# Kernel optimization log

Hardware: AMD Instinct MI355X
Metric: run time of the kernel (lower is better)

The kernel has to match this reference:

```python
import jax, jax.numpy as jnp
import numpy as np

N = 100000      # nodes
E = 1600000     # edges (avg degree 16)
F_IN = 256
F_OUT = 128


def setup_inputs() -> dict:
    key = jax.random.key(0)
    k1, k2, k3, k4, k5 = jax.random.split(key, 5)
    x = jax.random.normal(k1, (N, F_IN), dtype=jnp.float32)
    adj_row = jax.random.randint(k2, (E,), 0, N, dtype=jnp.int32)
    adj_col = jax.random.randint(k3, (E,), 0, N, dtype=jnp.int32)
    adj_vals = jax.random.uniform(k4, (E,), dtype=jnp.float32)
    # he_uniform init for weight, zeros for bias (as in build())
    limit = jnp.sqrt(6.0 / F_IN)
    w = jax.random.uniform(k5, (F_IN, F_OUT), minval=-limit, maxval=limit, dtype=jnp.float32)
    b = jnp.zeros((F_OUT,), dtype=jnp.float32)
    return {"x": x, "adj_row": adj_row, "adj_col": adj_col, "adj_vals": adj_vals, "w": w, "b": b}


def reference(x, adj_row, adj_col, adj_vals, w, b):
    # dense feature transform: [N, F_in] @ [F_in, F_out] -> [N, F_out]
    h = x @ w
    # sparse adjacency SpMM (COO): out[r] += vals[e] * h[c] for edge e=(r,c)
    msgs = adj_vals[:, None] * h[adj_col]            # [E, F_out]
    agg = jax.ops.segment_sum(msgs, adj_row, num_segments=N)  # [N, F_out]
    # bias + relu activation
    return jax.nn.relu(agg + b)
```

## Files before the change

kernel.cpp:

```cpp
#include <hip/hip_runtime.h>
#include <hip/hip_bf16.h>
#include <cstdint>
#include <cstddef>

#define N_NODES 100000
#define N_EDGES 1600000
#define F_IN 256
#define F_OUT 128

#define NB 1563
#define NBLK 196
#define TILE 8192
#define CAP 1536

typedef __attribute__((ext_vector_type(8))) short short8;
typedef __attribute__((ext_vector_type(4))) float floatx4;

static __device__ __forceinline__ unsigned short f2bf(float f) {
    union { float f; unsigned u; } v; v.f = f;
    unsigned r = v.u + 0x7FFF + ((v.u >> 16) & 1);
    return (unsigned short)(r >> 16);
}

__global__ void prep_w(const float* __restrict__ w, unsigned short* __restrict__ wT) {
    int i = blockIdx.x * 256 + threadIdx.x;
    int k = i >> 7;
    int n = i & 127;
    int g = (k >> 3) ^ (n & 7);
    wT[n * 256 + g * 8 + (k & 7)] = f2bf(w[i]);
}

__global__ __launch_bounds__(256, 2) void gemm_xw(const float* __restrict__ x,
                                                  const unsigned short* __restrict__ wT,
                                                  unsigned short* __restrict__ h) {
    __shared__ __align__(16) unsigned short wlds[128 * 256];
    const int tid = threadIdx.x;
    {
        const floatx4* src = reinterpret_cast<const floatx4*>(wT);
        floatx4* dst = reinterpret_cast<floatx4*>(wlds);
        #pragma unroll
        for (int i = 0; i < 16; i++) dst[tid + i * 256] = src[tid + i * 256];
    }
    __syncthreads();

    const int wave = tid >> 6, lane = tid & 63;
    const int quad = lane >> 4, l16 = lane & 15;
    const int rowbase = blockIdx.x * 256 + wave * 64;

    floatx4 acc[4][8];
    #pragma unroll
    for (int mf = 0; mf < 4; mf++)
        #pragma unroll
        for (int nt = 0; nt < 8; nt++) acc[mf][nt] = (floatx4)0.f;

    #pragma unroll
    for (int ks = 0; ks < 8; ks++) {
        const int k0 = ks * 32 + quad * 8;
        short8 afrag[4];
        #pragma unroll
        for (int mf = 0; mf < 4; mf++) {
            int row = rowbase + mf * 16 + l16;
            if (row >= N_NODES) row = N_NODES - 1;
            const float* xp = x + (size_t)row * F_IN + k0;
            floatx4 x0 = *reinterpret_cast<const floatx4*>(xp);
            floatx4 x1 = *reinterpret_cast<const floatx4*>(xp + 4);
            short8 a;
            a[0] = (short)f2bf(x0[0]); a[1] = (short)f2bf(x0[1]);
            a[2] = (short)f2bf(x0[2]); a[3] = (short)f2bf(x0[3]);
            a[4] = (short)f2bf(x1[0]); a[5] = (short)f2bf(x1[1]);
            a[6] = (short)f2bf(x1[2]); a[7] = (short)f2bf(x1[3]);
            afrag[mf] = a;
        }
        short8 bfrag[8];
        const int gq = ks * 4 + quad;
        #pragma unroll
        for (int nt = 0; nt < 8; nt++) {
            const int n = nt * 16 + l16;
            const int g = gq ^ (n & 7);
            bfrag[nt] = *reinterpret_cast<const short8*>(&wlds[n * 256 + g * 8]);
        }
        #pragma unroll
        for (int mf = 0; mf < 4; mf++)
            #pragma unroll
            for (int nt = 0; nt < 8; nt++)
                acc[mf][nt] = __builtin_amdgcn_mfma_f32_16x16x32_bf16(
                    afrag[mf], bfrag[nt], acc[mf][nt], 0, 0, 0);
    }

    #pragma unroll
    for (int mf = 0; mf < 4; mf++) {
        const int mbase = rowbase + mf * 16 + quad * 4;
        #pragma unroll
        for (int reg = 0; reg < 4; reg++) {
            const int m = mbase + reg;
            if (m < N_NODES) {
                short8 hv;
                #pragma unroll
                for (int nt = 0; nt < 8; nt++) hv[nt] = (short)f2bf(acc[mf][nt][reg]);
                *reinterpret_cast<short8*>(&h[(size_t)m * F_OUT + l16 * 8]) = hv;
            }
        }
    }
}

__global__ __launch_bounds__(256) void bucket_hist(const int* __restrict__ row,
                                                   int* __restrict__ bucket_total,
                                                   int* __restrict__ blockbase) {
    __shared__ int hist[NB];
    const int t = threadIdx.x, blk = blockIdx.x;
    for (int i = t; i < NB; i += 256) hist[i] = 0;
    __syncthreads();
    const long tb = (long)blk * TILE;
    #pragma unroll
    for (int c = 0; c < 8; c++) {
        long i0 = tb + c * 1024 + t * 4;
        if (i0 + 4 <= N_EDGES) {
            int4 r = *reinterpret_cast<const int4*>(row + i0);
            atomicAdd(&hist[r.x >> 6], 1); atomicAdd(&hist[r.y >> 6], 1);
            atomicAdd(&hist[r.z >> 6], 1); atomicAdd(&hist[r.w >> 6], 1);
        } else {
            for (long i = i0; i < N_EDGES && i < i0 + 4; i++)
                atomicAdd(&hist[row[i] >> 6], 1);
        }
    }
    __syncthreads();
    for (int bin = t; bin < NB; bin += 256)
        blockbase[bin * NBLK + blk] = atomicAdd(&bucket_total[bin], hist[bin]);
}

__global__ void bucket_scan(const int* __restrict__ bucket_total,
                            int* __restrict__ bucket_base) {
    const int lane = threadIdx.x;
    int loc[25];
    int s = 0;
    #pragma unroll
    for (int k = 0; k < 25; k++) {
        int idx = lane * 25 + k;
        int v = (idx < NB) ? bucket_total[idx] : 0;
        loc[k] = s; s += v;
    }
    int run = s;
    #pragma unroll
    for (int off = 1; off < 64; off <<= 1) {
        int u = __shfl_up(run, off);
        if (lane >= off) run += u;
    }
    const int base = run - s;
    #pragma unroll
    for (int k = 0; k < 25; k++) {
        int idx = lane * 25 + k;
        if (idx <= NB) bucket_base[idx] = base + loc[k];
    }
}

__global__ __launch_bounds__(256) void bucket_scatter(const int* __restrict__ row,
                                                      const int* __restrict__ col,
                                                      const float* __restrict__ val,
                                                      const int* __restrict__ bucket_base,
                                                      const int* __restrict__ blockbase,
                                                      int2* __restrict__ metabuf) {
    __shared__ int sbase[NB];
    const int t = threadIdx.x, blk = blockIdx.x;
    for (int bin = t; bin < NB; bin += 256)
        sbase[bin] = bucket_base[bin] + blockbase[bin * NBLK + blk];
    __syncthreads();
    const long tb = (long)blk * TILE;
    #pragma unroll
    for (int c = 0; c < 8; c++) {
        long i0 = tb + c * 1024 + t * 4;
        if (i0 + 4 <= N_EDGES) {
            int4 r  = *reinterpret_cast<const int4*>(row + i0);
            int4 cc = *reinterpret_cast<const int4*>(col + i0);
            floatx4 vv = *reinterpret_cast<const floatx4*>(val + i0);
            int rr[4] = {r.x, r.y, r.z, r.w};
            int c4[4] = {cc.x, cc.y, cc.z, cc.w};
            float v4[4] = {vv[0], vv[1], vv[2], vv[3]};
            #pragma unroll
            for (int j = 0; j < 4; j++) {
                int bin = rr[j] >> 6, rl = rr[j] & 63;
                int pos = atomicAdd(&sbase[bin], 1);
                metabuf[pos] = make_int2(c4[j] | (rl << 24), __float_as_int(v4[j]));
            }
        } else {
            for (long i = i0; i < N_EDGES && i < i0 + 4; i++) {
                int rv = row[i];
                int bin = rv >> 6, rl = rv & 63;
                int pos = atomicAdd(&sbase[bin], 1);
                metabuf[pos] = make_int2(col[i] | (rl << 24), __float_as_int(val[i]));
            }
        }
    }
}

__global__ __launch_bounds__(512, 8) void spmm_fused(const unsigned short* __restrict__ h,
                                                     const int* __restrict__ bucket_base,
                                                     const int2* __restrict__ meta,
                                                     const float* __restrict__ bias,
                                                     float* __restrict__ out) {
    __shared__ int2 raw[CAP];
    __shared__ int2 ord[CAP];
    __shared__ int hist[64], startS[64], cursor[64];
    const int t = threadIdx.x, b = blockIdx.x;
    const int b0 = bucket_base[b];
    int n = bucket_base[b + 1] - b0; if (n > CAP) n = CAP;

    if (t < 64) hist[t] = 0;
    __syncthreads();
    for (int i = t; i < n; i += 512) {
        int2 e = meta[b0 + i];
        raw[i] = e;
        atomicAdd(&hist[((unsigned)e.x >> 24) & 63], 1);
    }
    __syncthreads();
    if (t < 64) {
        int h0 = hist[t];
        int s0 = h0;
        #pragma unroll
        for (int off = 1; off < 64; off <<= 1) {
            int u = __shfl_up(s0, off);
            if (t >= off) s0 += u;
        }
        startS[t] = s0 - h0; cursor[t] = s0 - h0;
    }
    __syncthreads();
    for (int i = t; i < n; i += 512) {
        int2 e = raw[i];
        int rl = ((unsigned)e.x >> 24) & 63;
        int pos = atomicAdd(&cursor[rl], 1);
        ord[pos] = make_int2(e.x & 0x00FFFFFF, e.y);
    }
    __syncthreads();

    const int lane = t & 63;
    const int l16 = lane & 15;
    const int grp = (t >> 6) * 4 + (lane >> 4);
    const unsigned short* hp = h + l16 * 8;

    #pragma unroll
    for (int j = 0; j < 2; j++) {
        const int rl = grp * 2 + j;
        const int s = startS[rl], d = hist[rl];
        float acc[8];
        #pragma unroll
        for (int k = 0; k < 8; k++) acc[k] = 0.f;
        for (int i = 0; i < d; i += 4) {
            int2 mm[4];
            #pragma unroll
            for (int u = 0; u < 4; u++) {
                int idx = i + u; if (idx > d - 1) idx = d - 1;
                mm[u] = ord[s + idx];
            }
            uint4 hv[4];
            #pragma unroll
            for (int u = 0; u < 4; u++)
                hv[u] = *reinterpret_cast<const uint4*>(hp + (size_t)mm[u].x * F_OUT);
            #pragma unroll
            for (int u = 0; u < 4; u++) {
                float v = (i + u < d) ? __int_as_float(mm[u].y) : 0.f;
                #pragma unroll
                for (int k = 0; k < 4; k++) {
                    unsigned uu = ((const unsigned*)&hv[u])[k];
                    acc[2 * k]     += v * __uint_as_float(uu << 16);
                    acc[2 * k + 1] += v * __uint_as_float(uu & 0xffff0000u);
                }
            }
        }
        const int r = b * 64 + rl;
        if (r < N_NODES) {
            float* op = out + (size_t)r * F_OUT + l16;
            #pragma unroll
            for (int jc = 0; jc < 8; jc++) {
                float o = fmaxf(acc[jc] + bias[jc * 16 + l16], 0.f);
                op[jc * 16] = o;
            }
        }
    }
}

extern "C" void kernel_launch(void* const* d_in, const int* in_sizes, int n_in,
                              void* d_out, int out_size, void* d_ws, size_t ws_size,
                              hipStream_t stream) {
    const float* x        = (const float*)d_in[0];
    const int*   adj_row  = (const int*)d_in[1];
    const int*   adj_col  = (const int*)d_in[2];
    const float* adj_vals = (const float*)d_in[3];
    const float* w        = (const float*)d_in[4];
    const float* b        = (const float*)d_in[5];
    float* out = (float*)d_out;

    char* ws = (char*)d_ws;
    unsigned short* wT = (unsigned short*)ws;
    unsigned short* h  = (unsigned short*)(ws + 65536);
    size_t off = 65536 + (size_t)N_NODES * F_OUT * 2;
    int2* metabuf  = (int2*)(ws + off);   off += (size_t)N_EDGES * 8;
    int* blockbase = (int*)(ws + off);    off += (size_t)NB * NBLK * 4;
    int* bucket_total = (int*)(ws + off); off += 8192;
    int* bucket_base  = (int*)(ws + off); off += 8192;

    prep_w<<<128, 256, 0, stream>>>(w, wT);
    hipMemsetAsync(bucket_total, 0, NB * 4, stream);
    gemm_xw<<<(N_NODES + 255) / 256, 256, 0, stream>>>(x, wT, h);
    bucket_hist<<<NBLK, 256, 0, stream>>>(adj_row, bucket_total, blockbase);
    bucket_scan<<<1, 64, 0, stream>>>(bucket_total, bucket_base);
    bucket_scatter<<<NBLK, 256, 0, stream>>>(adj_row, adj_col, adj_vals,
                                             bucket_base, blockbase, metabuf);
    spmm_fused<<<NB, 512, 0, stream>>>(h, bucket_base, metabuf, b, out);
}
```

Baseline: 304.3 us.

## Fuse GEMM and edge bucketing into one launch with fixed-capacity buckets

Replaces the separate gemm, histogram, scan and scatter kernels with one launch. The first blocks run the X·W GEMM and the remaining blocks histogram and scatter edges. Buckets now have a fixed capacity slot (CAP entries each), so the global prefix scan and per-block base table go away, and the counter reset moves into prep_w, removing the memset. This saves several launches and serialization points and lets the GEMM and the bucketing overlap. The trade-off is a larger, padded metadata buffer, and edges beyond CAP per bucket are silently dropped, though the old spmm kernel already clamped to CAP.

```diff
diff --git a/kernel.cpp b/kernel.cpp
--- a/kernel.cpp
+++ b/kernel.cpp
@@ -12,6 +12,7 @@
 #define NBLK 196
 #define TILE 8192
 #define CAP 1536
+#define GEMM_BLOCKS 391
 
 typedef __attribute__((ext_vector_type(8))) short short8;
 typedef __attribute__((ext_vector_type(4))) float floatx4;
@@ -22,178 +23,155 @@
     return (unsigned short)(r >> 16);
 }
 
-__global__ void prep_w(const float* __restrict__ w, unsigned short* __restrict__ wT) {
+__global__ void prep_w(const float* __restrict__ w, unsigned short* __restrict__ wT,
+                       int* __restrict__ cnt) {
     int i = blockIdx.x * 256 + threadIdx.x;
     int k = i >> 7;
     int n = i & 127;
     int g = (k >> 3) ^ (n & 7);
     wT[n * 256 + g * 8 + (k & 7)] = f2bf(w[i]);
-}
-
-__global__ __launch_bounds__(256, 2) void gemm_xw(const float* __restrict__ x,
-                                                  const unsigned short* __restrict__ wT,
-                                                  unsigned short* __restrict__ h) {
-    __shared__ __align__(16) unsigned short wlds[128 * 256];
+    if (blockIdx.x == 0)
+        for (int j = threadIdx.x; j < NB; j += 256) cnt[j] = 0;
+}
+
+__global__ __launch_bounds__(256, 2) void fused_mid(const float* __restrict__ x,
+                                                    const unsigned short* __restrict__ wT,
+                                                    unsigned short* __restrict__ h,
+                                                    const int* __restrict__ row,
+                                                    const int* __restrict__ col,
+                                                    const float* __restrict__ val,
+                                                    int* __restrict__ cnt,
+                                                    int2* __restrict__ metabuf) {
+    __shared__ __align__(16) unsigned short smem[128 * 256];
     const int tid = threadIdx.x;
-    {
-        const floatx4* src = reinterpret_cast<const floatx4*>(wT);
-        floatx4* dst = reinterpret_cast<floatx4*>(wlds);
-        #pragma unroll
-        for (int i = 0; i < 16; i++) dst[tid + i * 256] = src[tid + i * 256];
-    }
-    __syncthreads();
-
-    const int wave = tid >> 6, lane = tid & 63;
-    const int quad = lane >> 4, l16 = lane & 15;
-    const int rowbase = blockIdx.x * 256 + wave * 64;
-
-    floatx4 acc[4][8];
-    #pragma unroll
-    for (int mf = 0; mf < 4; mf++)
-        #pragma unroll
-        for (int nt = 0; nt < 8; nt++) acc[mf][nt] = (floatx4)0.f;
-
-    #pragma unroll
-    for (int ks = 0; ks < 8; ks++) {
-        const int k0 = ks * 32 + quad * 8;
-        short8 afrag[4];
+
+    if (blockIdx.x < GEMM_BLOCKS) {
+        unsigned short* wlds = smem;
+        {
+            const floatx4* src = reinterpret_cast<const floatx4*>(wT);
+            floatx4* dst = reinterpret_cast<floatx4*>(wlds);
+            #pragma unroll
+            for (int i = 0; i < 16; i++) dst[tid + i * 256] = src[tid + i * 256];
+        }
+        __syncthreads();
+
+        const int wave = tid >> 6, lane = tid & 63;
+        const int quad = lane >> 4, l16 = lane & 15;
+        const int rowbase = blockIdx.x * 256 + wave * 64;
+
+        floatx4 acc[4][8];
+        #pragma unroll
+        for (int mf = 0; mf < 4; mf++)
+            #pragma unroll
+            for (int nt = 0; nt < 8; nt++) acc[mf][nt] = (floatx4)0.f;
+
+        #pragma unroll
+        for (int ks = 0; ks < 8; ks++) {
+            const int k0 = ks * 32 + quad * 8;
+            short8 afrag[4];
+            #pragma unroll
+            for (int mf = 0; mf < 4; mf++) {
+                int r = rowbase + mf * 16 + l16;
+                if (r >= N_NODES) r = N_NODES - 1;
+                const float* xp = x + (size_t)r * F_IN + k0;
+                floatx4 x0 = *reinterpret_cast<const floatx4*>(xp);
+                floatx4 x1 = *reinterpret_cast<const floatx4*>(xp + 4);
+                short8 a;
+                a[0] = (short)f2bf(x0[0]); a[1] = (short)f2bf(x0[1]);
+                a[2] = (short)f2bf(x0[2]); a[3] = (short)f2bf(x0[3]);
+                a[4] = (short)f2bf(x1[0]); a[5] = (short)f2bf(x1[1]);
+                a[6] = (short)f2bf(x1[2]); a[7] = (short)f2bf(x1[3]);
+                afrag[mf] = a;
+            }
+            short8 bfrag[8];
+            const int gq = ks * 4 + quad;
+            #pragma unroll
+            for (int nt = 0; nt < 8; nt++) {
+                const int n = nt * 16 + l16;
+                const int g = gq ^ (n & 7);
+                bfrag[nt] = *reinterpret_cast<const short8*>(&wlds[n * 256 + g * 8]);
+            }
+            #pragma unroll
+            for (int mf = 0; mf < 4; mf++)
+                #pragma unroll
+                for (int nt = 0; nt < 8; nt++)
+                    acc[mf][nt] = __builtin_amdgcn_mfma_f32_16x16x32_bf16(
+                        afrag[mf], bfrag[nt], acc[mf][nt], 0, 0, 0);
+        }
+
         #pragma unroll
         for (int mf = 0; mf < 4; mf++) {
-            int row = rowbase + mf * 16 + l16;
-            if (row >= N_NODES) row = N_NODES - 1;
-            const float* xp = x + (size_t)row * F_IN + k0;
-            floatx4 x0 = *reinterpret_cast<const floatx4*>(xp);
-            floatx4 x1 = *reinterpret_cast<const floatx4*>(xp + 4);
-            short8 a;
-            a[0] = (short)f2bf(x0[0]); a[1] = (short)f2bf(x0[1]);
-            a[2] = (short)f2bf(x0[2]); a[3] = (short)f2bf(x0[3]);
-            a[4] = (short)f2bf(x1[0]); a[5] = (short)f2bf(x1[1]);
-            a[6] = (short)f2bf(x1[2]); a[7] = (short)f2bf(x1[3]);
-            afrag[mf] = a;
-        }
-        short8 bfrag[8];
-        const int gq = ks * 4 + quad;
-        #pragma unroll
-        for (int nt = 0; nt < 8; nt++) {
-            const int n = nt * 16 + l16;
-            const int g = gq ^ (n & 7);
-            bfrag[nt] = *reinterpret_cast<const short8*>(&wlds[n * 256 + g * 8]);
-        }
-        #pragma unroll
-        for (int mf = 0; mf < 4; mf++)
-            #pragma unroll
-            for (int nt = 0; nt < 8; nt++)
-                acc[mf][nt] = __builtin_amdgcn_mfma_f32_16x16x32_bf16(
-                    afrag[mf], bfrag[nt], acc[mf][nt], 0, 0, 0);
-    }
-
-    #pragma unroll
-    for (int mf = 0; mf < 4; mf++) {
-        const int mbase = rowbase + mf * 16 + quad * 4;
-        #pragma unroll
-        for (int reg = 0; reg < 4; reg++) {
-            const int m = mbase + reg;
-            if (m < N_NODES) {
-                short8 hv;
+            const int mbase = rowbase + mf * 16 + quad * 4;
+            #pragma unroll
+            for (int reg = 0; reg < 4; reg++) {
+                const int m = mbase + reg;
+                if (m < N_NODES) {
+                    short8 hv;
+                    #pragma unroll
+                    for (int nt = 0; nt < 8; nt++) hv[nt] = (short)f2bf(acc[mf][nt][reg]);
+                    *reinterpret_cast<short8*>(&h[(size_t)m * F_OUT + l16 * 8]) = hv;
+                }
+            }
+        }
+    } else {
+        int* hist   = reinterpret_cast<int*>(smem);
+        int* cursor = hist + NB;
+        const int blk = blockIdx.x - GEMM_BLOCKS;
+        for (int i = tid; i < NB; i += 256) hist[i] = 0;
+        __syncthreads();
+        const long tb = (long)blk * TILE;
+        #pragma unroll
+        for (int c = 0; c < 8; c++) {
+            long i0 = tb + c * 1024 + tid * 4;
+            if (i0 + 4 <= N_EDGES) {
+                int4 r = *reinterpret_cast<const int4*>(row + i0);
+                atomicAdd(&hist[r.x >> 6], 1); atomicAdd(&hist[r.y >> 6], 1);
+                atomicAdd(&hist[r.z >> 6], 1); atomicAdd(&hist[r.w >> 6], 1);
+            } else {
+                for (long i = i0; i < N_EDGES && i < i0 + 4; i++)
+                    atomicAdd(&hist[row[i] >> 6], 1);
+            }
+        }
+        __syncthreads();
+        for (int bin = tid; bin < NB; bin += 256) {
+            int hc = hist[bin];
+            int base = bin * CAP;
+            if (hc) base += atomicAdd(&cnt[bin], hc);
+            cursor[bin] = base;
+        }
+        __syncthreads();
+        #pragma unroll
+        for (int c = 0; c < 8; c++) {
+            long i0 = tb + c * 1024 + tid * 4;
+            if (i0 + 4 <= N_EDGES) {
+                int4 r  = *reinterpret_cast<const int4*>(row + i0);
+                int4 cc = *reinterpret_cast<const int4*>(col + i0);
+                floatx4 vv = *reinterpret_cast<const floatx4*>(val + i0);
+                int rr[4] = {r.x, r.y, r.z, r.w};
+                int c4[4] = {cc.x, cc.y, cc.z, cc.w};
+                float v4[4] = {vv[0], vv[1], vv[2], vv[3]};
                 #pragma unroll
-                for (int nt = 0; nt < 8; nt++) hv[nt] = (short)f2bf(acc[mf][nt][reg]);
-                *reinterpret_cast<short8*>(&h[(size_t)m * F_OUT + l16 * 8]) = hv;
-            }
-        }
-    }
-}
-
-__global__ __launch_bounds__(256) void bucket_hist(const int* __restrict__ row,
-                                                   int* __restrict__ bucket_total,
-                                                   int* __restrict__ blockbase) {
-    __shared__ int hist[NB];
-    const int t = threadIdx.x, blk = blockIdx.x;
-    for (int i = t; i < NB; i += 256) hist[i] = 0;
-    __syncthreads();
-    const long tb = (long)blk * TILE;
-    #pragma unroll
-    for (int c = 0; c < 8; c++) {
-        long i0 = tb + c * 1024 + t * 4;
-        if (i0 + 4 <= N_EDGES) {
-            int4 r = *reinterpret_cast<const int4*>(row + i0);
-            atomicAdd(&hist[r.x >> 6], 1); atomicAdd(&hist[r.y >> 6], 1);
-            atomicAdd(&hist[r.z >> 6], 1); atomicAdd(&hist[r.w >> 6], 1);
-        } else {
-            for (long i = i0; i < N_EDGES && i < i0 + 4; i++)
-                atomicAdd(&hist[row[i] >> 6], 1);
-        }
-    }
-    __syncthreads();
-    for (int bin = t; bin < NB; bin += 256)
-        blockbase[bin * NBLK + blk] = atomicAdd(&bucket_total[bin], hist[bin]);
-}
-
-__global__ void bucket_scan(const int* __restrict__ bucket_total,
-                            int* __restrict__ bucket_base) {
-    const int lane = threadIdx.x;
-    int loc[25];
-    int s = 0;
-    #pragma unroll
-    for (int k = 0; k < 25; k++) {
-        int idx = lane * 25 + k;
-        int v = (idx < NB) ? bucket_total[idx] : 0;
-        loc[k] = s; s += v;
-    }
-    int run = s;
-    #pragma unroll
-    for (int off = 1; off < 64; off <<= 1) {
-        int u = __shfl_up(run, off);
-        if (lane >= off) run += u;
-    }
-    const int base = run - s;
-    #pragma unroll
-    for (int k = 0; k < 25; k++) {
-        int idx = lane * 25 + k;
-        if (idx <= NB) bucket_base[idx] = base + loc[k];
-    }
-}
-
-__global__ __launch_bounds__(256) void bucket_scatter(const int* __restrict__ row,
-                                                      const int* __restrict__ col,
-                                                      const float* __restrict__ val,
-                                                      const int* __restrict__ bucket_base,
-                                                      const int* __restrict__ blockbase,
-                                                      int2* __restrict__ metabuf) {
-    __shared__ int sbase[NB];
-    const int t = threadIdx.x, blk = blockIdx.x;
-    for (int bin = t; bin < NB; bin += 256)
-        sbase[bin] = bucket_base[bin] + blockbase[bin * NBLK + blk];
-    __syncthreads();
-    const long tb = (long)blk * TILE;
-    #pragma unroll
-    for (int c = 0; c < 8; c++) {
-        long i0 = tb + c * 1024 + t * 4;
-        if (i0 + 4 <= N_EDGES) {
-            int4 r  = *reinterpret_cast<const int4*>(row + i0);
-            int4 cc = *reinterpret_cast<const int4*>(col + i0);
-            floatx4 vv = *reinterpret_cast<const floatx4*>(val + i0);
-            int rr[4] = {r.x, r.y, r.z, r.w};
-            int c4[4] = {cc.x, cc.y, cc.z, cc.w};
-            float v4[4] = {vv[0], vv[1], vv[2], vv[3]};
-            #pragma unroll
-            for (int j = 0; j < 4; j++) {
-                int bin = rr[j] >> 6, rl = rr[j] & 63;
-                int pos = atomicAdd(&sbase[bin], 1);
-                metabuf[pos] = make_int2(c4[j] | (rl << 24), __float_as_int(v4[j]));
-            }
-        } else {
-            for (long i = i0; i < N_EDGES && i < i0 + 4; i++) {
-                int rv = row[i];
-                int bin = rv >> 6, rl = rv & 63;
-                int pos = atomicAdd(&sbase[bin], 1);
-                metabuf[pos] = make_int2(col[i] | (rl << 24), __float_as_int(val[i]));
+                for (int j = 0; j < 4; j++) {
+                    int bin = rr[j] >> 6, rl = rr[j] & 63;
+                    int pos = atomicAdd(&cursor[bin], 1);
+                    if (pos < (bin + 1) * CAP)
+                        metabuf[pos] = make_int2(c4[j] | (rl << 24), __float_as_int(v4[j]));
+                }
+            } else {
+                for (long i = i0; i < N_EDGES && i < i0 + 4; i++) {
+                    int rv = row[i];
+                    int bin = rv >> 6, rl = rv & 63;
+                    int pos = atomicAdd(&cursor[bin], 1);
+                    if (pos < (bin + 1) * CAP)
+                        metabuf[pos] = make_int2(col[i] | (rl << 24), __float_as_int(val[i]));
+                }
             }
         }
     }
 }
 
 __global__ __launch_bounds__(512, 8) void spmm_fused(const unsigned short* __restrict__ h,
-                                                     const int* __restrict__ bucket_base,
+                                                     const int* __restrict__ cnt,
                                                      const int2* __restrict__ meta,
                                                      const float* __restrict__ bias,
                                                      float* __restrict__ out) {
@@ -201,8 +179,8 @@
     __shared__ int2 ord[CAP];
     __shared__ int hist[64], startS[64], cursor[64];
     const int t = threadIdx.x, b = blockIdx.x;
-    const int b0 = bucket_base[b];
-    int n = bucket_base[b + 1] - b0; if (n > CAP) n = CAP;
+    const int b0 = b * CAP;
+    int n = cnt[b]; if (n > CAP) n = CAP;
 
     if (t < 64) hist[t] = 0;
     __syncthreads();
@@ -292,17 +270,11 @@
     unsigned short* wT = (unsigned short*)ws;
     unsigned short* h  = (unsigned short*)(ws + 65536);
     size_t off = 65536 + (size_t)N_NODES * F_OUT * 2;
-    int2* metabuf  = (int2*)(ws + off);   off += (size_t)N_EDGES * 8;
-    int* blockbase = (int*)(ws + off);    off += (size_t)NB * NBLK * 4;
-    int* bucket_total = (int*)(ws + off); off += 8192;
-    int* bucket_base  = (int*)(ws + off); off += 8192;
-
-    prep_w<<<128, 256, 0, stream>>>(w, wT);
-    hipMemsetAsync(bucket_total, 0, NB * 4, stream);
-    gemm_xw<<<(N_NODES + 255) / 256, 256, 0, stream>>>(x, wT, h);
-    bucket_hist<<<NBLK, 256, 0, stream>>>(adj_row, bucket_total, blockbase);
-    bucket_scan<<<1, 64, 0, stream>>>(bucket_total, bucket_base);
-    bucket_scatter<<<NBLK, 256, 0, stream>>>(adj_row, adj_col, adj_vals,
-                                             bucket_base, blockbase, metabuf);
-    spmm_fused<<<NB, 512, 0, stream>>>(h, bucket_base, metabuf, b, out);
-}
+    int2* metabuf = (int2*)(ws + off);  off += (size_t)NB * CAP * 8;
+    int* cnt      = (int*)(ws + off);   off += 8192;
+
+    prep_w<<<128, 256, 0, stream>>>(w, wT, cnt);
+    fused_mid<<<GEMM_BLOCKS + NBLK, 256, 0, stream>>>(x, wT, h, adj_row, adj_col,
+                                                      adj_vals, cnt, metabuf);
+    spmm_fused<<<NB, 512, 0, stream>>>(h, cnt, metabuf, b, out);
+}
```

Result: faster. 287.8 us (-5.4%).
